# Kernel tuning notes

Measured on AMD Instinct MI355X. Metric: run time of the kernel, lower is better.

## Reference

```python
import jax, jax.numpy as jnp
import numpy as np

N = 50000
IN_DIM = 1024
HID = 64
HEADS = 4
OUT_DIM = 128
NEG_SLOPE = 0.2


def setup_inputs() -> dict:
    key = jax.random.key(0)
    ks = jax.random.split(key, 10)
    x = jax.random.normal(ks[0], (N, IN_DIM), dtype=jnp.float32)
    edge_index = jax.random.randint(ks[1], (2, 800000), 0, N, dtype=jnp.int64)
    # GATConv 1: input_dim -> hidden_dim, heads=HEADS, concat=True
    W1 = jax.random.normal(ks[2], (IN_DIM, HEADS * HID), dtype=jnp.float32) * (1.0 / np.sqrt(IN_DIM))
    att_src1 = jax.random.normal(ks[3], (HEADS, HID), dtype=jnp.float32) * 0.1
    att_dst1 = jax.random.normal(ks[4], (HEADS, HID), dtype=jnp.float32) * 0.1
    b1 = jnp.zeros((HEADS * HID,), dtype=jnp.float32)
    # GATConv 2: hidden_dim*heads -> output_dim, heads=1, concat=False
    W2 = jax.random.normal(ks[5], (HEADS * HID, OUT_DIM), dtype=jnp.float32) * (1.0 / np.sqrt(HEADS * HID))
    att_src2 = jax.random.normal(ks[6], (1, OUT_DIM), dtype=jnp.float32) * 0.1
    att_dst2 = jax.random.normal(ks[7], (1, OUT_DIM), dtype=jnp.float32) * 0.1
    b2 = jnp.zeros((OUT_DIM,), dtype=jnp.float32)
    return {"x": x, "edge_index": edge_index, "W1": W1, "att_src1": att_src1,
            "att_dst1": att_dst1, "b1": b1, "W2": W2, "att_src2": att_src2,
            "att_dst2": att_dst2, "b2": b2}


def _gat_conv(x, src, dst, W, a_src, a_dst, b, heads, concat):
    # x: [N, F_in]; src/dst: [E'] (self-loops already included)
    n = x.shape[0]
    h = (x @ W).reshape(n, heads, -1)                 # [N, H, D]
    # per-node attention halves (PyG style)
    alpha_s = jnp.sum(h * a_src[None], axis=-1)       # [N, H]
    alpha_d = jnp.sum(h * a_dst[None], axis=-1)       # [N, H]
    e = jax.nn.leaky_relu(alpha_s[src] + alpha_d[dst], NEG_SLOPE)  # [E', H]
    # segment softmax over incoming edges of each destination node
    m = jax.ops.segment_max(e, dst, num_segments=n)   # [N, H]
    m = jnp.where(jnp.isfinite(m), m, 0.0)
    e = jnp.exp(e - m[dst])
    s = jax.ops.segment_sum(e, dst, num_segments=n)   # [N, H]
    alpha = e / (s[dst] + 1e-16)                      # [E', H]
    out = jax.ops.segment_sum(h[src] * alpha[:, :, None], dst, num_segments=n)  # [N, H, D]
    out = out.reshape(n, -1) if concat else out.mean(axis=1)
    return out + b


def reference(x, edge_index, W1, att_src1, att_dst1, b1, W2, att_src2, att_dst2, b2):
    n = x.shape[0]
    # PyG GATConv default: add self-loops
    loops = jnp.arange(n, dtype=edge_index.dtype)
    src = jnp.concatenate([edge_index[0], loops])
    dst = jnp.concatenate([edge_index[1], loops])
    # dropout layers are identity in eval mode
    h = _gat_conv(x, src, dst, W1, att_src1, att_dst1, b1, HEADS, concat=True)
    h = jax.nn.elu(h)
    out = _gat_conv(h, src, dst, W2, att_src2, att_dst2, b2, 1, concat=False)
    # F.normalize(p=2, dim=-1)
    norm = jnp.maximum(jnp.linalg.norm(out, axis=-1, keepdims=True), 1e-12)
    return out / norm
```

## Files before the change

kernel.cpp:

```cpp
#include <hip/hip_runtime.h>
#include <math.h>

#define NNODES 50000
#define E0 800000
#define ETOT 850000
#define IN_DIM 1024
#define HEADS 4
#define C1 256
#define C2 128
#define NEG_SLOPE 0.2f

typedef short bf16x8 __attribute__((ext_vector_type(8)));
typedef float f32x4 __attribute__((ext_vector_type(4)));
typedef unsigned short ushort_t;

__device__ __forceinline__ void edge_sd(const int* __restrict__ ei, int e, int& s, int& d) {
    if (e < E0) { s = ei[e]; d = ei[E0 + e]; }
    else        { s = e - E0; d = s; }
}

__device__ __forceinline__ ushort_t f2b(float f) {
    unsigned u = __float_as_uint(f);
    return (ushort_t)((u + 0x7fffu + ((u >> 16) & 1u)) >> 16);
}
__device__ __forceinline__ float bf2f(ushort_t u) {
    return __uint_as_float((unsigned)u << 16);
}
__device__ __forceinline__ float lrelu(float v) { return v > 0.f ? v : NEG_SLOPE * v; }

__device__ __forceinline__ void gload_lds16(const void* g, void* l) {
    __builtin_amdgcn_global_load_lds(
        (const __attribute__((address_space(1))) unsigned int*)g,
        (__attribute__((address_space(3))) unsigned int*)l, 16, 0, 0);
}

__device__ __forceinline__ bf16x8 cvt_bf8(float4 f0, float4 f1) {
    bf16x8 p;
    p[0] = f2b(f0.x); p[1] = f2b(f0.y); p[2] = f2b(f0.z); p[3] = f2b(f0.w);
    p[4] = f2b(f1.x); p[5] = f2b(f1.y); p[6] = f2b(f1.z); p[7] = f2b(f1.w);
    return p;
}

__global__ __launch_bounds__(256) void wtrans_kernel(const float* __restrict__ W,
                                                     ushort_t* __restrict__ WT,
                                                     int K, int N)
{
    int idx = blockIdx.x * 256 + threadIdx.x;
    if (idx >= K * N) return;
    int k = idx / N, n = idx % N;
    WT[((size_t)(k >> 3) * N + n) * 8 + (k & 7)] = f2b(W[idx]);
}

__global__ __launch_bounds__(256, 4) void gemm_fb(const float* __restrict__ A,
                                                  const ushort_t* __restrict__ Bblk,
                                                  ushort_t* __restrict__ Cb,
                                                  int M, int N, int K)
{
    __shared__ __align__(16) ushort_t Bs[2][8 * 128 * 8];

    const int tid  = threadIdx.x;
    const int lane = tid & 63;
    const int wid  = tid >> 6;
    const int wr   = wid >> 1, wc = wid & 1;
    const int rowBase = blockIdx.y * 64;
    const int colBase = blockIdx.x * 128;
    const int r0 = lane & 15;
    const int kh = lane >> 4;

    const float* aP0 = A + (size_t)min(rowBase + wr * 32 + r0,      M - 1) * K + kh * 8;
    const float* aP1 = A + (size_t)min(rowBase + wr * 32 + 16 + r0, M - 1) * K + kh * 8;

    const int p0 = wid * 2;
    const ushort_t* bsrc0 = Bblk + ((size_t)(p0 + 0) * N + colBase + lane) * 8;
    const ushort_t* bsrc1 = Bblk + ((size_t)(p0 + 1) * N + colBase + lane) * 8;
    const int bdst0 = (p0 + 0) * 1024;
    const int bdst1 = (p0 + 1) * 1024;
    const size_t bstep = (size_t)8 * N * 8;

    const int brd = (wc * 64 + r0) * 8;

    f32x4 zero = {0.f, 0.f, 0.f, 0.f};
    f32x4 acc[2][4];
    #pragma unroll
    for (int i = 0; i < 2; ++i)
        #pragma unroll
        for (int j = 0; j < 4; ++j) acc[i][j] = zero;

    gload_lds16(bsrc0,       &Bs[0][bdst0]);
    gload_lds16(bsrc0 + 512, &Bs[0][bdst0 + 512]);
    gload_lds16(bsrc1,       &Bs[0][bdst1]);
    gload_lds16(bsrc1 + 512, &Bs[0][bdst1 + 512]);
    float4 n00 = *(const float4*)(aP0 +  0), n01 = *(const float4*)(aP0 +  4);
    float4 n02 = *(const float4*)(aP0 + 32), n03 = *(const float4*)(aP0 + 36);
    float4 n10 = *(const float4*)(aP1 +  0), n11 = *(const float4*)(aP1 +  4);
    float4 n12 = *(const float4*)(aP1 + 32), n13 = *(const float4*)(aP1 + 36);
    __syncthreads();

    const ushort_t* rdB = Bs[0];
    ushort_t*       stB = Bs[1];

    bf16x8 aC[2][2];
    aC[0][0] = cvt_bf8(n00, n01); aC[0][1] = cvt_bf8(n02, n03);
    aC[1][0] = cvt_bf8(n10, n11); aC[1][1] = cvt_bf8(n12, n13);

    const int nt = K >> 6;
    for (int t = 0; t < nt; ++t) {
        const int kt = (t + 1) << 6;
        const bool has_next = kt < K;
        if (has_next) {
            const ushort_t* b0 = bsrc0 + (size_t)(t + 1) * bstep;
            const ushort_t* b1 = bsrc1 + (size_t)(t + 1) * bstep;
            gload_lds16(b0,       stB + bdst0);
            gload_lds16(b0 + 512, stB + bdst0 + 512);
            gload_lds16(b1,       stB + bdst1);
            gload_lds16(b1 + 512, stB + bdst1 + 512);
            n00 = *(const float4*)(aP0 + kt +  0); n01 = *(const float4*)(aP0 + kt +  4);
            n02 = *(const float4*)(aP0 + kt + 32); n03 = *(const float4*)(aP0 + kt + 36);
            n10 = *(const float4*)(aP1 + kt +  0); n11 = *(const float4*)(aP1 + kt +  4);
            n12 = *(const float4*)(aP1 + kt + 32); n13 = *(const float4*)(aP1 + kt + 36);
        }

        #pragma unroll
        for (int kc = 0; kc < 2; ++kc) {
            const ushort_t* bbase = rdB + (kc * 4 + kh) * 1024 + brd;
            bf16x8 bF[4];
            #pragma unroll
            for (int fj = 0; fj < 4; ++fj) bF[fj] = *(const bf16x8*)(bbase + fj * 128);
            #pragma unroll
            for (int fi = 0; fi < 2; ++fi)
                #pragma unroll
                for (int fj = 0; fj < 4; ++fj)
                    acc[fi][fj] = __builtin_amdgcn_mfma_f32_16x16x32_bf16(
                        aC[fi][kc], bF[fj], acc[fi][fj], 0, 0, 0);
        }

        if (has_next) {
            aC[0][0] = cvt_bf8(n00, n01); aC[0][1] = cvt_bf8(n02, n03);
            aC[1][0] = cvt_bf8(n10, n11); aC[1][1] = cvt_bf8(n12, n13);
        }
        __syncthreads();
        ushort_t* tmp = (ushort_t*)rdB; rdB = stB; stB = tmp;
    }

    #pragma unroll
    for (int fi = 0; fi < 2; ++fi) {
        int row0 = rowBase + wr * 32 + fi * 16 + kh * 4;
        #pragma unroll
        for (int i = 0; i < 4; ++i) {
            int row = row0 + i;
            if (row < M) {
                #pragma unroll
                for (int fj = 0; fj < 4; ++fj)
                    Cb[(size_t)row * N + colBase + wc * 64 + fj * 16 + r0] = f2b(acc[fi][fj][i]);
            }
        }
    }
}

__global__ __launch_bounds__(256, 4) void gemm_bb(const ushort_t* __restrict__ Ab,
                                                  const ushort_t* __restrict__ Bblk,
                                                  ushort_t* __restrict__ Cb,
                                                  int M, int N, int K)
{
    __shared__ __align__(16) ushort_t Bs[2][8 * 128 * 8];

    const int tid  = threadIdx.x;
    const int lane = tid & 63;
    const int wid  = tid >> 6;
    const int wr   = wid >> 1, wc = wid & 1;
    const int rowBase = blockIdx.y * 64;
    const int colBase = blockIdx.x * 128;
    const int r0 = lane & 15;
    const int kh = lane >> 4;

    const ushort_t* aP0 = Ab + (size_t)min(rowBase + wr * 32 + r0,      M - 1) * K + kh * 8;
    const ushort_t* aP1 = Ab + (size_t)min(rowBase + wr * 32 + 16 + r0, M - 1) * K + kh * 8;

    const int p0 = wid * 2;
    const ushort_t* bsrc0 = Bblk + ((size_t)(p0 + 0) * N + colBase + lane) * 8;
    const ushort_t* bsrc1 = Bblk + ((size_t)(p0 + 1) * N + colBase + lane) * 8;
    const int bdst0 = (p0 + 0) * 1024;
    const int bdst1 = (p0 + 1) * 1024;
    const size_t bstep = (size_t)8 * N * 8;

    const int brd = (wc * 64 + r0) * 8;

    f32x4 zero = {0.f, 0.f, 0.f, 0.f};
    f32x4 acc[2][4];
    #pragma unroll
    for (int i = 0; i < 2; ++i)
        #pragma unroll
        for (int j = 0; j < 4; ++j) acc[i][j] = zero;

    gload_lds16(bsrc0,       &Bs[0][bdst0]);
    gload_lds16(bsrc0 + 512, &Bs[0][bdst0 + 512]);
    gload_lds16(bsrc1,       &Bs[0][bdst1]);
    gload_lds16(bsrc1 + 512, &Bs[0][bdst1 + 512]);
    bf16x8 aC[2][2], aN[2][2];
    aC[0][0] = *(const bf16x8*)(aP0 +  0); aC[0][1] = *(const bf16x8*)(aP0 + 32);
    aC[1][0] = *(const bf16x8*)(aP1 +  0); aC[1][1] = *(const bf16x8*)(aP1 + 32);
    __syncthreads();

    const ushort_t* rdB = Bs[0];
    ushort_t*       stB = Bs[1];

    const int nt = K >> 6;
    for (int t = 0; t < nt; ++t) {
        const int kt = (t + 1) << 6;
        const bool has_next = kt < K;
        if (has_next) {
            const ushort_t* b0 = bsrc0 + (size_t)(t + 1) * bstep;
            const ushort_t* b1 = bsrc1 + (size_t)(t + 1) * bstep;
            gload_lds16(b0,       stB + bdst0);
            gload_lds16(b0 + 512, stB + bdst0 + 512);
            gload_lds16(b1,       stB + bdst1);
            gload_lds16(b1 + 512, stB + bdst1 + 512);
            aN[0][0] = *(const bf16x8*)(aP0 + kt +  0); aN[0][1] = *(const bf16x8*)(aP0 + kt + 32);
            aN[1][0] = *(const bf16x8*)(aP1 + kt +  0); aN[1][1] = *(const bf16x8*)(aP1 + kt + 32);
        }

        #pragma unroll
        for (int kc = 0; kc < 2; ++kc) {
            const ushort_t* bbase = rdB + (kc * 4 + kh) * 1024 + brd;
            bf16x8 bF[4];
            #pragma unroll
            for (int fj = 0; fj < 4; ++fj) bF[fj] = *(const bf16x8*)(bbase + fj * 128);
            #pragma unroll
            for (int fi = 0; fi < 2; ++fi)
                #pragma unroll
                for (int fj = 0; fj < 4; ++fj)
                    acc[fi][fj] = __builtin_amdgcn_mfma_f32_16x16x32_bf16(
                        aC[fi][kc], bF[fj], acc[fi][fj], 0, 0, 0);
        }

        if (has_next) {
            aC[0][0] = aN[0][0]; aC[0][1] = aN[0][1];
            aC[1][0] = aN[1][0]; aC[1][1] = aN[1][1];
        }
        __syncthreads();
        ushort_t* tmp = (ushort_t*)rdB; rdB = stB; stB = tmp;
    }

    #pragma unroll
    for (int fi = 0; fi < 2; ++fi) {
        int row0 = rowBase + wr * 32 + fi * 16 + kh * 4;
        #pragma unroll
        for (int i = 0; i < 4; ++i) {
            int row = row0 + i;
            if (row < M) {
                #pragma unroll
                for (int fj = 0; fj < 4; ++fj)
                    Cb[(size_t)row * N + colBase + wc * 64 + fj * 16 + r0] = f2b(acc[fi][fj][i]);
            }
        }
    }
}

__global__ __launch_bounds__(256) void alpha1_kernel(const ushort_t* __restrict__ h1b,
                                                     const float* __restrict__ asrc,
                                                     const float* __restrict__ adst,
                                                     float* __restrict__ out_s,
                                                     float* __restrict__ out_d)
{
    int n = blockIdx.x;
    int t = threadIdx.x;
    float h = bf2f(h1b[(size_t)n * C1 + t]);
    float s = h * asrc[t];
    float d = h * adst[t];
    #pragma unroll
    for (int off = 32; off > 0; off >>= 1) {
        s += __shfl_down(s, off);
        d += __shfl_down(d, off);
    }
    if ((t & 63) == 0) {
        out_s[n * HEADS + (t >> 6)] = s;
        out_d[n * HEADS + (t >> 6)] = d;
    }
}

__global__ __launch_bounds__(64) void alpha2_kernel(const ushort_t* __restrict__ h2b,
                                                    const float* __restrict__ asrc,
                                                    const float* __restrict__ adst,
                                                    float* __restrict__ out_s,
                                                    float* __restrict__ out_d)
{
    int n = blockIdx.x;
    int t = threadIdx.x;
    float a = bf2f(h2b[(size_t)n * C2 + t]);
    float b = bf2f(h2b[(size_t)n * C2 + t + 64]);
    float s = a * asrc[t] + b * asrc[t + 64];
    float d = a * adst[t] + b * adst[t + 64];
    #pragma unroll
    for (int off = 32; off > 0; off >>= 1) {
        s += __shfl_down(s, off);
        d += __shfl_down(d, off);
    }
    if (t == 0) { out_s[n] = s; out_d[n] = d; }
}

__global__ __launch_bounds__(256) void deg_kernel(const int* __restrict__ ei,
                                                  int* __restrict__ deg)
{
    int e = blockIdx.x * blockDim.x + threadIdx.x;
    if (e >= ETOT) return;
    int s, d; edge_sd(ei, e, s, d);
    atomicAdd(&deg[d], 1);
}

#define SCAN_T 1024
__global__ __launch_bounds__(SCAN_T) void scan_kernel(const int* __restrict__ deg,
                                                      int* __restrict__ rowptr)
{
    __shared__ int wsum[16];
    __shared__ int chunk_tot;
    __shared__ int carry_s;
    const int t = threadIdx.x, lane = t & 63, w = t >> 6;
    if (t == 0) carry_s = 0;
    __syncthreads();
    for (int base = 0; base < NNODES; base += SCAN_T * 4) {
        int idx = base + t * 4;
        int v0 = (idx + 0 < NNODES) ? deg[idx + 0] : 0;
        int v1 = (idx + 1 < NNODES) ? deg[idx + 1] : 0;
        int v2 = (idx + 2 < NNODES) ? deg[idx + 2] : 0;
        int v3 = (idx + 3 < NNODES) ? deg[idx + 3] : 0;
        int p0 = v0, p1 = p0 + v1, p2 = p1 + v2, p3 = p2 + v3;
        int incl = p3;
        #pragma unroll
        for (int off = 1; off < 64; off <<= 1) {
            int nb = __shfl_up(incl, off);
            if (lane >= off) incl += nb;
        }
        if (lane == 63) wsum[w] = incl;
        __syncthreads();
        if (w == 0 && lane < 16) {
            int ws = wsum[lane];
            int wincl = ws;
            #pragma unroll
            for (int off = 1; off < 16; off <<= 1) {
                int nb = __shfl_up(wincl, off);
                if (lane >= off) wincl += nb;
            }
            wsum[lane] = wincl - ws;
            if (lane == 15) chunk_tot = wincl;
        }
        __syncthreads();
        int carry = carry_s;
        int basev = carry + wsum[w] + (incl - p3);
        if (idx + 0 < NNODES) rowptr[idx + 0] = basev;
        if (idx + 1 < NNODES) rowptr[idx + 1] = basev + p0;
        if (idx + 2 < NNODES) rowptr[idx + 2] = basev + p1;
        if (idx + 3 < NNODES) rowptr[idx + 3] = basev + p2;
        __syncthreads();
        if (t == 0) carry_s = carry + chunk_tot;
        __syncthreads();
    }
    if (threadIdx.x == 0) rowptr[NNODES] = carry_s;
}

__global__ __launch_bounds__(256) void scatter_kernel(const int* __restrict__ ei,
                                                      int* __restrict__ cursor,
                                                      int* __restrict__ srcs)
{
    int e = blockIdx.x * blockDim.x + threadIdx.x;
    if (e >= ETOT) return;
    int s, d; edge_sd(ei, e, s, d);
    int pos = atomicAdd(&cursor[d], 1);
    srcs[pos] = s;
}

__global__ __launch_bounds__(256) void weights1_kernel(const int* __restrict__ rowptr,
                                                       const int* __restrict__ srcs,
                                                       const float4* __restrict__ as1,
                                                       const float4* __restrict__ ad1,
                                                       float4* __restrict__ wbuf)
{
    int d = blockIdx.x * 4 + (threadIdx.x >> 6);
    if (d >= NNODES) return;
    int lane = threadIdx.x & 63;
    int beg = rowptr[d], end = rowptr[d + 1];
    float4 adv = ad1[d];
    float m0 = -INFINITY, m1 = -INFINITY, m2 = -INFINITY, m3 = -INFINITY;
    for (int i = beg + lane; i < end; i += 64) {
        int s = srcs[i];
        float4 av = as1[s];
        m0 = fmaxf(m0, lrelu(av.x + adv.x));
        m1 = fmaxf(m1, lrelu(av.y + adv.y));
        m2 = fmaxf(m2, lrelu(av.z + adv.z));
        m3 = fmaxf(m3, lrelu(av.w + adv.w));
    }
    #pragma unroll
    for (int off = 32; off > 0; off >>= 1) {
        m0 = fmaxf(m0, __shfl_xor(m0, off));
        m1 = fmaxf(m1, __shfl_xor(m1, off));
        m2 = fmaxf(m2, __shfl_xor(m2, off));
        m3 = fmaxf(m3, __shfl_xor(m3, off));
    }
    float s0 = 0.f, s1 = 0.f, s2 = 0.f, s3 = 0.f;
    for (int i = beg + lane; i < end; i += 64) {
        int s = srcs[i];
        float4 av = as1[s];
        float w0 = expf(lrelu(av.x + adv.x) - m0);
        float w1 = expf(lrelu(av.y + adv.y) - m1);
        float w2 = expf(lrelu(av.z + adv.z) - m2);
        float w3 = expf(lrelu(av.w + adv.w) - m3);
        wbuf[i] = make_float4(w0, w1, w2, w3);
        s0 += w0; s1 += w1; s2 += w2; s3 += w3;
    }
    #pragma unroll
    for (int off = 32; off > 0; off >>= 1) {
        s0 += __shfl_xor(s0, off);
        s1 += __shfl_xor(s1, off);
        s2 += __shfl_xor(s2, off);
        s3 += __shfl_xor(s3, off);
    }
    float i0 = 1.f / (s0 + 1e-16f), i1 = 1.f / (s1 + 1e-16f);
    float i2 = 1.f / (s2 + 1e-16f), i3 = 1.f / (s3 + 1e-16f);
    for (int i = beg + lane; i < end; i += 64) {
        float4 wv = wbuf[i];
        wbuf[i] = make_float4(wv.x * i0, wv.y * i1, wv.z * i2, wv.w * i3);
    }
}

__global__ __launch_bounds__(256) void weights2_kernel(const int* __restrict__ rowptr,
                                                       const int* __restrict__ srcs,
                                                       const float* __restrict__ as2,
                                                       const float* __restrict__ ad2,
                                                       float* __restrict__ wbuf)
{
    int d = blockIdx.x * 4 + (threadIdx.x >> 6);
    if (d >= NNODES) return;
    int lane = threadIdx.x & 63;
    int beg = rowptr[d], end = rowptr[d + 1];
    float adv = ad2[d];
    float m = -INFINITY;
    for (int i = beg + lane; i < end; i += 64)
        m = fmaxf(m, lrelu(as2[srcs[i]] + adv));
    #pragma unroll
    for (int off = 32; off > 0; off >>= 1) m = fmaxf(m, __shfl_xor(m, off));
    float sm = 0.f;
    for (int i = beg + lane; i < end; i += 64) {
        float w = expf(lrelu(as2[srcs[i]] + adv) - m);
        wbuf[i] = w;
        sm += w;
    }
    #pragma unroll
    for (int off = 32; off > 0; off >>= 1) sm += __shfl_xor(sm, off);
    float inv = 1.f / (sm + 1e-16f);
    for (int i = beg + lane; i < end; i += 64) wbuf[i] *= inv;
}

__global__ __launch_bounds__(256) void aggr1_csr(const int* __restrict__ rowptr,
                                                 const int* __restrict__ srcs,
                                                 const ushort_t* __restrict__ h1b,
                                                 const float* __restrict__ wbuf,
                                                 const float* __restrict__ b1,
                                                 ushort_t* __restrict__ out)
{
    int d = blockIdx.x * 4 + (threadIdx.x >> 6);
    if (d >= NNODES) return;
    int lane = threadIdx.x & 63;
    int c0 = lane * 4;
    int head = lane >> 4;
    int beg = rowptr[d], end = rowptr[d + 1];
    float a0 = 0.f, a1 = 0.f, a2 = 0.f, a3 = 0.f;
    int i = beg;
    for (; i + 1 < end; i += 2) {
        int s0 = srcs[i], s1 = srcs[i + 1];
        float w0 = wbuf[i * 4 + head], w1 = wbuf[i * 4 + 4 + head];
        ushort4 v0 = *(const ushort4*)(h1b + (size_t)s0 * C1 + c0);
        ushort4 v1 = *(const ushort4*)(h1b + (size_t)s1 * C1 + c0);
        a0 = fmaf(w0, bf2f(v0.x), a0); a1 = fmaf(w0, bf2f(v0.y), a1);
        a2 = fmaf(w0, bf2f(v0.z), a2); a3 = fmaf(w0, bf2f(v0.w), a3);
        a0 = fmaf(w1, bf2f(v1.x), a0); a1 = fmaf(w1, bf2f(v1.y), a1);
        a2 = fmaf(w1, bf2f(v1.z), a2); a3 = fmaf(w1, bf2f(v1.w), a3);
    }
    if (i < end) {
        int s0 = srcs[i];
        float w0 = wbuf[i * 4 + head];
        ushort4 v0 = *(const ushort4*)(h1b + (size_t)s0 * C1 + c0);
        a0 = fmaf(w0, bf2f(v0.x), a0); a1 = fmaf(w0, bf2f(v0.y), a1);
        a2 = fmaf(w0, bf2f(v0.z), a2); a3 = fmaf(w0, bf2f(v0.w), a3);
    }
    float4 bv = *(const float4*)(b1 + c0);
    float o0 = a0 + bv.x, o1 = a1 + bv.y, o2 = a2 + bv.z, o3 = a3 + bv.w;
    ushort4 r;
    r.x = f2b(o0 > 0.f ? o0 : (expf(o0) - 1.f));
    r.y = f2b(o1 > 0.f ? o1 : (expf(o1) - 1.f));
    r.z = f2b(o2 > 0.f ? o2 : (expf(o2) - 1.f));
    r.w = f2b(o3 > 0.f ? o3 : (expf(o3) - 1.f));
    *(ushort4*)(out + (size_t)d * C1 + c0) = r;
}

__global__ __launch_bounds__(256) void aggr2_csr(const int* __restrict__ rowptr,
                                                 const int* __restrict__ srcs,
                                                 const ushort_t* __restrict__ h2b,
                                                 const float* __restrict__ wbuf,
                                                 const float* __restrict__ b2,
                                                 float* __restrict__ out)
{
    int d = blockIdx.x * 4 + (threadIdx.x >> 6);
    if (d >= NNODES) return;
    int lane = threadIdx.x & 63;
    int c0 = lane * 2;
    int beg = rowptr[d], end = rowptr[d + 1];
    float a0 = 0.f, a1 = 0.f;
    int i = beg;
    for (; i + 1 < end; i += 2) {
        int s0 = srcs[i], s1 = srcs[i + 1];
        float w0 = wbuf[i], w1 = wbuf[i + 1];
        ushort2 v0 = *(const ushort2*)(h2b + (size_t)s0 * C2 + c0);
        ushort2 v1 = *(const ushort2*)(h2b + (size_t)s1 * C2 + c0);
        a0 = fmaf(w0, bf2f(v0.x), a0); a1 = fmaf(w0, bf2f(v0.y), a1);
        a0 = fmaf(w1, bf2f(v1.x), a0); a1 = fmaf(w1, bf2f(v1.y), a1);
    }
    if (i < end) {
        float w0 = wbuf[i];
        ushort2 v0 = *(const ushort2*)(h2b + (size_t)srcs[i] * C2 + c0);
        a0 = fmaf(w0, bf2f(v0.x), a0); a1 = fmaf(w0, bf2f(v0.y), a1);
    }
    float2 bv = *(const float2*)(b2 + c0);
    float o0 = a0 + bv.x, o1 = a1 + bv.y;
    float sq = o0 * o0 + o1 * o1;
    #pragma unroll
    for (int off = 32; off > 0; off >>= 1) sq += __shfl_xor(sq, off);
    float inv = 1.0f / fmaxf(sqrtf(sq), 1e-12f);
    float2 r = make_float2(o0 * inv, o1 * inv);
    *(float2*)(out + (size_t)d * C2 + c0) = r;
}

extern "C" void kernel_launch(void* const* d_in, const int* in_sizes, int n_in,
                              void* d_out, int out_size, void* d_ws, size_t ws_size,
                              hipStream_t stream)
{
    const float* x     = (const float*)d_in[0];
    const int*   ei    = (const int*)d_in[1];
    const float* W1    = (const float*)d_in[2];
    const float* asrc1 = (const float*)d_in[3];
    const float* adst1 = (const float*)d_in[4];
    const float* b1    = (const float*)d_in[5];
    const float* W2    = (const float*)d_in[6];
    const float* asrc2 = (const float*)d_in[7];
    const float* adst2 = (const float*)d_in[8];
    const float* b2    = (const float*)d_in[9];
    float* out = (float*)d_out;

    char* ws = (char*)d_ws;
    size_t off = 0;
    auto alloc = [&](size_t nbytes) {
        void* p = ws + off;
        off += (nbytes + 15) & ~(size_t)15;
        return p;
    };
    ushort_t* h1b    = (ushort_t*)alloc((size_t)NNODES * C1 * 2);
    ushort_t* act1b  = (ushort_t*)alloc((size_t)NNODES * C1 * 2);
    ushort_t* h2b    = (ushort_t*)alloc((size_t)NNODES * C2 * 2);
    ushort_t* W1blk  = (ushort_t*)alloc((size_t)C1 * IN_DIM * 2);
    ushort_t* W2blk  = (ushort_t*)alloc((size_t)C2 * C1 * 2);
    float*    as1    = (float*)alloc((size_t)NNODES * HEADS * 4);
    float*    ad1    = (float*)alloc((size_t)NNODES * HEADS * 4);
    float*    as2    = (float*)alloc((size_t)NNODES * 4);
    float*    ad2    = (float*)alloc((size_t)NNODES * 4);
    float*    wbuf1  = (float*)alloc((size_t)ETOT * HEADS * 4);
    float*    wbuf2  = (float*)alloc((size_t)ETOT * 4);
    int*      deg    = (int*)alloc((size_t)NNODES * 4);
    int*      rowptr = (int*)alloc((size_t)(NNODES + 1) * 4);
    int*      cursor = (int*)alloc((size_t)(NNODES + 1) * 4);
    int*      srcs   = (int*)alloc((size_t)ETOT * 4);

    const int eb = (ETOT + 255) / 256;
    const int nb4 = (NNODES + 3) / 4;

    wtrans_kernel<<<(IN_DIM * C1 + 255) / 256, 256, 0, stream>>>(W1, W1blk, IN_DIM, C1);
    wtrans_kernel<<<(C1 * C2 + 255) / 256, 256, 0, stream>>>(W2, W2blk, C1, C2);

    hipMemsetAsync(deg, 0, (size_t)NNODES * 4, stream);
    deg_kernel<<<eb, 256, 0, stream>>>(ei, deg);
    scan_kernel<<<1, SCAN_T, 0, stream>>>(deg, rowptr);
    hipMemcpyAsync(cursor, rowptr, (size_t)(NNODES + 1) * 4, hipMemcpyDeviceToDevice, stream);
    scatter_kernel<<<eb, 256, 0, stream>>>(ei, cursor, srcs);

    dim3 g1(C1 / 128, (NNODES + 63) / 64);
    gemm_fb<<<g1, 256, 0, stream>>>(x, W1blk, h1b, NNODES, C1, IN_DIM);
    alpha1_kernel<<<NNODES, 256, 0, stream>>>(h1b, asrc1, adst1, as1, ad1);
    weights1_kernel<<<nb4, 256, 0, stream>>>(rowptr, srcs, (const float4*)as1,
                                             (const float4*)ad1, (float4*)wbuf1);
    aggr1_csr<<<nb4, 256, 0, stream>>>(rowptr, srcs, h1b, wbuf1, b1, act1b);

    dim3 g2(C2 / 128, (NNODES + 63) / 64);
    gemm_bb<<<g2, 256, 0, stream>>>(act1b, W2blk, h2b, NNODES, C2, C1);
    alpha2_kernel<<<NNODES, 64, 0, stream>>>(h2b, asrc2, adst2, as2, ad2);
    weights2_kernel<<<nb4, 256, 0, stream>>>(rowptr, srcs, as2, ad2, wbuf2);
    aggr2_csr<<<nb4, 256, 0, stream>>>(rowptr, srcs, h2b, wbuf2, b2, out);
}
```

Before: 491.4 us.

## Triple-buffer B tiles and prefetch two K-steps ahead in fp32 GEMM

Replaces the double-buffered loop in gemm_fb with a three-stage LDS ring and two register sets of A, issuing loads two iterations ahead. Partial vmcnt waits and a raw s_barrier replace the full __syncthreads, so loads for step t+1 can stay in flight during compute. This costs more LDS and registers, so launch bounds drop occupancy from 4 to 3 blocks. The hand-placed vmcnt counts depend on exact load ordering, and a raw s_barrier without an LDS waitcnt could be fragile.

```diff
diff --git a/kernel.cpp b/kernel.cpp
--- a/kernel.cpp
+++ b/kernel.cpp
@@ -51,12 +51,12 @@
     WT[((size_t)(k >> 3) * N + n) * 8 + (k & 7)] = f2b(W[idx]);
 }
 
-__global__ __launch_bounds__(256, 4) void gemm_fb(const float* __restrict__ A,
+__global__ __launch_bounds__(256, 3) void gemm_fb(const float* __restrict__ A,
                                                   const ushort_t* __restrict__ Bblk,
                                                   ushort_t* __restrict__ Cb,
                                                   int M, int N, int K)
 {
-    __shared__ __align__(16) ushort_t Bs[2][8 * 128 * 8];
+    __shared__ __align__(16) ushort_t Bs[3][8 * 128 * 8];
 
     const int tid  = threadIdx.x;
     const int lane = tid & 63;
@@ -86,61 +86,86 @@
         #pragma unroll
         for (int j = 0; j < 4; ++j) acc[i][j] = zero;
 
-    gload_lds16(bsrc0,       &Bs[0][bdst0]);
-    gload_lds16(bsrc0 + 512, &Bs[0][bdst0 + 512]);
-    gload_lds16(bsrc1,       &Bs[0][bdst1]);
-    gload_lds16(bsrc1 + 512, &Bs[0][bdst1 + 512]);
-    float4 n00 = *(const float4*)(aP0 +  0), n01 = *(const float4*)(aP0 +  4);
-    float4 n02 = *(const float4*)(aP0 + 32), n03 = *(const float4*)(aP0 + 36);
-    float4 n10 = *(const float4*)(aP1 +  0), n11 = *(const float4*)(aP1 +  4);
-    float4 n12 = *(const float4*)(aP1 + 32), n13 = *(const float4*)(aP1 + 36);
-    __syncthreads();
-
-    const ushort_t* rdB = Bs[0];
-    ushort_t*       stB = Bs[1];
-
-    bf16x8 aC[2][2];
-    aC[0][0] = cvt_bf8(n00, n01); aC[0][1] = cvt_bf8(n02, n03);
-    aC[1][0] = cvt_bf8(n10, n11); aC[1][1] = cvt_bf8(n12, n13);
-
+    ushort_t* pCur = Bs[0];
+    ushort_t* pNxt = Bs[1];
+    ushort_t* pStg = Bs[2];
+
+    float4 ra[8], rb[8];
+    bf16x8 fA[2][2], fB[2][2];
     const int nt = K >> 6;
-    for (int t = 0; t < nt; ++t) {
-        const int kt = (t + 1) << 6;
-        const bool has_next = kt < K;
-        if (has_next) {
-            const ushort_t* b0 = bsrc0 + (size_t)(t + 1) * bstep;
-            const ushort_t* b1 = bsrc1 + (size_t)(t + 1) * bstep;
-            gload_lds16(b0,       stB + bdst0);
-            gload_lds16(b0 + 512, stB + bdst0 + 512);
-            gload_lds16(b1,       stB + bdst1);
-            gload_lds16(b1 + 512, stB + bdst1 + 512);
-            n00 = *(const float4*)(aP0 + kt +  0); n01 = *(const float4*)(aP0 + kt +  4);
-            n02 = *(const float4*)(aP0 + kt + 32); n03 = *(const float4*)(aP0 + kt + 36);
-            n10 = *(const float4*)(aP1 + kt +  0); n11 = *(const float4*)(aP1 + kt +  4);
-            n12 = *(const float4*)(aP1 + kt + 32); n13 = *(const float4*)(aP1 + kt + 36);
-        }
-
-        #pragma unroll
-        for (int kc = 0; kc < 2; ++kc) {
-            const ushort_t* bbase = rdB + (kc * 4 + kh) * 1024 + brd;
-            bf16x8 bF[4];
-            #pragma unroll
-            for (int fj = 0; fj < 4; ++fj) bF[fj] = *(const bf16x8*)(bbase + fj * 128);
-            #pragma unroll
-            for (int fi = 0; fi < 2; ++fi)
-                #pragma unroll
-                for (int fj = 0; fj < 4; ++fj)
-                    acc[fi][fj] = __builtin_amdgcn_mfma_f32_16x16x32_bf16(
-                        aC[fi][kc], bF[fj], acc[fi][fj], 0, 0, 0);
-        }
-
-        if (has_next) {
-            aC[0][0] = cvt_bf8(n00, n01); aC[0][1] = cvt_bf8(n02, n03);
-            aC[1][0] = cvt_bf8(n10, n11); aC[1][1] = cvt_bf8(n12, n13);
-        }
-        __syncthreads();
-        ushort_t* tmp = (ushort_t*)rdB; rdB = stB; stB = tmp;
-    }
+
+    gload_lds16(bsrc0,       pCur + bdst0);
+    gload_lds16(bsrc0 + 512, pCur + bdst0 + 512);
+    gload_lds16(bsrc1,       pCur + bdst1);
+    gload_lds16(bsrc1 + 512, pCur + bdst1 + 512);
+    ra[0] = *(const float4*)(aP0 +  0); ra[1] = *(const float4*)(aP0 +  4);
+    ra[2] = *(const float4*)(aP0 + 32); ra[3] = *(const float4*)(aP0 + 36);
+    ra[4] = *(const float4*)(aP1 +  0); ra[5] = *(const float4*)(aP1 +  4);
+    ra[6] = *(const float4*)(aP1 + 32); ra[7] = *(const float4*)(aP1 + 36);
+    {
+        const ushort_t* b0 = bsrc0 + bstep;
+        const ushort_t* b1 = bsrc1 + bstep;
+        gload_lds16(b0,       pNxt + bdst0);
+        gload_lds16(b0 + 512, pNxt + bdst0 + 512);
+        gload_lds16(b1,       pNxt + bdst1);
+        gload_lds16(b1 + 512, pNxt + bdst1 + 512);
+        rb[0] = *(const float4*)(aP0 + 64 +  0); rb[1] = *(const float4*)(aP0 + 64 +  4);
+        rb[2] = *(const float4*)(aP0 + 64 + 32); rb[3] = *(const float4*)(aP0 + 64 + 36);
+        rb[4] = *(const float4*)(aP1 + 64 +  0); rb[5] = *(const float4*)(aP1 + 64 +  4);
+        rb[6] = *(const float4*)(aP1 + 64 + 32); rb[7] = *(const float4*)(aP1 + 64 + 36);
+    }
+    asm volatile("s_waitcnt vmcnt(12)" ::: "memory");
+    fA[0][0] = cvt_bf8(ra[0], ra[1]); fA[0][1] = cvt_bf8(ra[2], ra[3]);
+    fA[1][0] = cvt_bf8(ra[4], ra[5]); fA[1][1] = cvt_bf8(ra[6], ra[7]);
+    __builtin_amdgcn_s_barrier();
+
+#define GEMM_STEP(T, RI, RC, FU, FF)                                            \
+    {                                                                           \
+        const int t2 = (T) + 2;                                                 \
+        const bool has2 = t2 < nt;                                              \
+        if (has2) {                                                             \
+            const ushort_t* b0 = bsrc0 + (size_t)t2 * bstep;                    \
+            const ushort_t* b1 = bsrc1 + (size_t)t2 * bstep;                    \
+            gload_lds16(b0,       pStg + bdst0);                                \
+            gload_lds16(b0 + 512, pStg + bdst0 + 512);                          \
+            gload_lds16(b1,       pStg + bdst1);                                \
+            gload_lds16(b1 + 512, pStg + bdst1 + 512);                          \
+            const float* a0 = aP0 + (t2 << 6);                                  \
+            const float* a1 = aP1 + (t2 << 6);                                  \
+            RI[0] = *(const float4*)(a0 +  0); RI[1] = *(const float4*)(a0 +  4);\
+            RI[2] = *(const float4*)(a0 + 32); RI[3] = *(const float4*)(a0 + 36);\
+            RI[4] = *(const float4*)(a1 +  0); RI[5] = *(const float4*)(a1 +  4);\
+            RI[6] = *(const float4*)(a1 + 32); RI[7] = *(const float4*)(a1 + 36);\
+        }                                                                       \
+        _Pragma("unroll")                                                       \
+        for (int kc = 0; kc < 2; ++kc) {                                        \
+            const ushort_t* bbase = pCur + (kc * 4 + kh) * 1024 + brd;          \
+            bf16x8 bF[4];                                                       \
+            _Pragma("unroll")                                                   \
+            for (int fj = 0; fj < 4; ++fj)                                      \
+                bF[fj] = *(const bf16x8*)(bbase + fj * 128);                    \
+            _Pragma("unroll")                                                   \
+            for (int fi = 0; fi < 2; ++fi)                                      \
+                _Pragma("unroll")                                               \
+                for (int fj = 0; fj < 4; ++fj)                                  \
+                    acc[fi][fj] = __builtin_amdgcn_mfma_f32_16x16x32_bf16(      \
+                        FU[fi][kc], bF[fj], acc[fi][fj], 0, 0, 0);              \
+        }                                                                       \
+        if ((T) + 1 < nt) {                                                     \
+            if (has2) asm volatile("s_waitcnt vmcnt(12)" ::: "memory");         \
+            else      asm volatile("s_waitcnt vmcnt(0)"  ::: "memory");         \
+            FF[0][0] = cvt_bf8(RC[0], RC[1]); FF[0][1] = cvt_bf8(RC[2], RC[3]); \
+            FF[1][0] = cvt_bf8(RC[4], RC[5]); FF[1][1] = cvt_bf8(RC[6], RC[7]); \
+            __builtin_amdgcn_s_barrier();                                       \
+        }                                                                       \
+        ushort_t* tmp = pCur; pCur = pNxt; pNxt = pStg; pStg = tmp;             \
+    }
+
+    for (int t = 0; t < nt; t += 2) {
+        GEMM_STEP(t,     ra, rb, fA, fB);
+        GEMM_STEP(t + 1, rb, ra, fB, fA);
+    }
+#undef GEMM_STEP
 
     #pragma unroll
     for (int fi = 0; fi < 2; ++fi) {
```

Result: slower. 510.0 us (+3.8%).

## Stage A tiles in LDS, read B directly from global; unroll CSR gathers by four

Applied to the files above, without the earlier changes.

Both GEMM kernels swap roles: the A operand is now loaded cooperatively in 256-wide K chunks, converted to bf16 and stored in LDS, while B fragments are read straight from global memory (and cache) instead of being staged via global_load_lds double buffering. This aims to coalesce the large fp32 A reads and cut per-k-step barriers, at the cost of a single-buffered LDS stage with two syncs per step, more registers (16 float4 staging), and occupancy lowered to 3. The aggregation kernels unroll the edge gather loop from 2 to 4 to keep more independent loads in flight.

```diff
diff --git a/kernel.cpp b/kernel.cpp
--- a/kernel.cpp
+++ b/kernel.cpp
@@ -28,12 +28,6 @@
 }
 __device__ __forceinline__ float lrelu(float v) { return v > 0.f ? v : NEG_SLOPE * v; }
 
-__device__ __forceinline__ void gload_lds16(const void* g, void* l) {
-    __builtin_amdgcn_global_load_lds(
-        (const __attribute__((address_space(1))) unsigned int*)g,
-        (__attribute__((address_space(3))) unsigned int*)l, 16, 0, 0);
-}
-
 __device__ __forceinline__ bf16x8 cvt_bf8(float4 f0, float4 f1) {
     bf16x8 p;
     p[0] = f2b(f0.x); p[1] = f2b(f0.y); p[2] = f2b(f0.z); p[3] = f2b(f0.w);
@@ -51,12 +45,12 @@
     WT[((size_t)(k >> 3) * N + n) * 8 + (k & 7)] = f2b(W[idx]);
 }
 
-__global__ __launch_bounds__(256, 4) void gemm_fb(const float* __restrict__ A,
+__global__ __launch_bounds__(256, 3) void gemm_fb(const float* __restrict__ A,
                                                   const ushort_t* __restrict__ Bblk,
                                                   ushort_t* __restrict__ Cb,
                                                   int M, int N, int K)
 {
-    __shared__ __align__(16) ushort_t Bs[2][8 * 128 * 8];
+    __shared__ __align__(16) ushort_t As[32 * 64 * 8];
 
     const int tid  = threadIdx.x;
     const int lane = tid & 63;
@@ -67,17 +61,14 @@
     const int r0 = lane & 15;
     const int kh = lane >> 4;
 
-    const float* aP0 = A + (size_t)min(rowBase + wr * 32 + r0,      M - 1) * K + kh * 8;
-    const float* aP1 = A + (size_t)min(rowBase + wr * 32 + 16 + r0, M - 1) * K + kh * 8;
-
-    const int p0 = wid * 2;
-    const ushort_t* bsrc0 = Bblk + ((size_t)(p0 + 0) * N + colBase + lane) * 8;
-    const ushort_t* bsrc1 = Bblk + ((size_t)(p0 + 1) * N + colBase + lane) * 8;
-    const int bdst0 = (p0 + 0) * 1024;
-    const int bdst1 = (p0 + 1) * 1024;
-    const size_t bstep = (size_t)8 * N * 8;
-
-    const int brd = (wc * 64 + r0) * 8;
+    const int srow = tid >> 2;
+    const int sq   = tid & 3;
+    const float* aSrc = A + (size_t)min(rowBase + srow, M - 1) * K + sq * 64;
+    ushort_t* aDst = As + (sq * 8) * 512 + srow * 8;
+
+    const ushort_t* bBase = Bblk + ((size_t)kh * N + colBase + wc * 64 + r0) * 8;
+
+    const ushort_t* aRd = As + kh * 512 + (wr * 32 + r0) * 8;
 
     f32x4 zero = {0.f, 0.f, 0.f, 0.f};
     f32x4 acc[2][4];
@@ -86,60 +77,39 @@
         #pragma unroll
         for (int j = 0; j < 4; ++j) acc[i][j] = zero;
 
-    gload_lds16(bsrc0,       &Bs[0][bdst0]);
-    gload_lds16(bsrc0 + 512, &Bs[0][bdst0 + 512]);
-    gload_lds16(bsrc1,       &Bs[0][bdst1]);
-    gload_lds16(bsrc1 + 512, &Bs[0][bdst1 + 512]);
-    float4 n00 = *(const float4*)(aP0 +  0), n01 = *(const float4*)(aP0 +  4);
-    float4 n02 = *(const float4*)(aP0 + 32), n03 = *(const float4*)(aP0 + 36);
-    float4 n10 = *(const float4*)(aP1 +  0), n11 = *(const float4*)(aP1 +  4);
-    float4 n12 = *(const float4*)(aP1 + 32), n13 = *(const float4*)(aP1 + 36);
-    __syncthreads();
-
-    const ushort_t* rdB = Bs[0];
-    ushort_t*       stB = Bs[1];
-
-    bf16x8 aC[2][2];
-    aC[0][0] = cvt_bf8(n00, n01); aC[0][1] = cvt_bf8(n02, n03);
-    aC[1][0] = cvt_bf8(n10, n11); aC[1][1] = cvt_bf8(n12, n13);
-
-    const int nt = K >> 6;
-    for (int t = 0; t < nt; ++t) {
-        const int kt = (t + 1) << 6;
-        const bool has_next = kt < K;
-        if (has_next) {
-            const ushort_t* b0 = bsrc0 + (size_t)(t + 1) * bstep;
-            const ushort_t* b1 = bsrc1 + (size_t)(t + 1) * bstep;
-            gload_lds16(b0,       stB + bdst0);
-            gload_lds16(b0 + 512, stB + bdst0 + 512);
-            gload_lds16(b1,       stB + bdst1);
-            gload_lds16(b1 + 512, stB + bdst1 + 512);
-            n00 = *(const float4*)(aP0 + kt +  0); n01 = *(const float4*)(aP0 + kt +  4);
-            n02 = *(const float4*)(aP0 + kt + 32); n03 = *(const float4*)(aP0 + kt + 36);
-            n10 = *(const float4*)(aP1 + kt +  0); n11 = *(const float4*)(aP1 + kt +  4);
-            n12 = *(const float4*)(aP1 + kt + 32); n13 = *(const float4*)(aP1 + kt + 36);
-        }
-
-        #pragma unroll
-        for (int kc = 0; kc < 2; ++kc) {
-            const ushort_t* bbase = rdB + (kc * 4 + kh) * 1024 + brd;
+    float4 st[16];
+    #pragma unroll
+    for (int i = 0; i < 16; ++i) st[i] = *(const float4*)(aSrc + i * 4);
+
+    const int nstep = K >> 8;
+    for (int s = 0; s < nstep; ++s) {
+        __syncthreads();
+        #pragma unroll
+        for (int j = 0; j < 8; ++j)
+            *(bf16x8*)(aDst + j * 512) = cvt_bf8(st[2 * j], st[2 * j + 1]);
+        __syncthreads();
+
+        if (s + 1 < nstep) {
+            const float* nsrc = aSrc + (size_t)(s + 1) * 256;
+            #pragma unroll
+            for (int i = 0; i < 16; ++i) st[i] = *(const float4*)(nsrc + i * 4);
+        }
+
+        #pragma unroll
+        for (int j = 0; j < 8; ++j) {
+            const ushort_t* bit = bBase + ((size_t)(s * 32 + j * 4) * N) * 8;
             bf16x8 bF[4];
             #pragma unroll
-            for (int fj = 0; fj < 4; ++fj) bF[fj] = *(const bf16x8*)(bbase + fj * 128);
-            #pragma unroll
-            for (int fi = 0; fi < 2; ++fi)
-                #pragma unroll
-                for (int fj = 0; fj < 4; ++fj)
-                    acc[fi][fj] = __builtin_amdgcn_mfma_f32_16x16x32_bf16(
-                        aC[fi][kc], bF[fj], acc[fi][fj], 0, 0, 0);
-        }
-
-        if (has_next) {
-            aC[0][0] = cvt_bf8(n00, n01); aC[0][1] = cvt_bf8(n02, n03);
-            aC[1][0] = cvt_bf8(n10, n11); aC[1][1] = cvt_bf8(n12, n13);
-        }
-        __syncthreads();
-        ushort_t* tmp = (ushort_t*)rdB; rdB = stB; stB = tmp;
+            for (int fj = 0; fj < 4; ++fj)
+                bF[fj] = *(const bf16x8*)(bit + (size_t)fj * 128);
+            bf16x8 aF0 = *(const bf16x8*)(aRd + j * 2048);
+            bf16x8 aF1 = *(const bf16x8*)(aRd + j * 2048 + 128);
+            #pragma unroll
+            for (int fj = 0; fj < 4; ++fj) {
+                acc[0][fj] = __builtin_amdgcn_mfma_f32_16x16x32_bf16(aF0, bF[fj], acc[0][fj], 0, 0, 0);
+                acc[1][fj] = __builtin_amdgcn_mfma_f32_16x16x32_bf16(aF1, bF[fj], acc[1][fj], 0, 0, 0);
+            }
+        }
     }
 
     #pragma unroll
@@ -162,7 +132,7 @@
                                                   ushort_t* __restrict__ Cb,
                                                   int M, int N, int K)
 {
-    __shared__ __align__(16) ushort_t Bs[2][8 * 128 * 8];
+    __shared__ __align__(16) ushort_t As[32 * 64 * 8];
 
     const int tid  = threadIdx.x;
     const int lane = tid & 63;
@@ -173,17 +143,13 @@
     const int r0 = lane & 15;
     const int kh = lane >> 4;
 
-    const ushort_t* aP0 = Ab + (size_t)min(rowBase + wr * 32 + r0,      M - 1) * K + kh * 8;
-    const ushort_t* aP1 = Ab + (size_t)min(rowBase + wr * 32 + 16 + r0, M - 1) * K + kh * 8;
-
-    const int p0 = wid * 2;
-    const ushort_t* bsrc0 = Bblk + ((size_t)(p0 + 0) * N + colBase + lane) * 8;
-    const ushort_t* bsrc1 = Bblk + ((size_t)(p0 + 1) * N + colBase + lane) * 8;
-    const int bdst0 = (p0 + 0) * 1024;
-    const int bdst1 = (p0 + 1) * 1024;
-    const size_t bstep = (size_t)8 * N * 8;
-
-    const int brd = (wc * 64 + r0) * 8;
+    const int srow = tid >> 2;
+    const int sq   = tid & 3;
+    const ushort_t* aSrc = Ab + (size_t)min(rowBase + srow, M - 1) * K + sq * 64;
+    ushort_t* aDst = As + (sq * 8) * 512 + srow * 8;
+
+    const ushort_t* bBase = Bblk + ((size_t)kh * N + colBase + wc * 64 + r0) * 8;
+    const ushort_t* aRd = As + kh * 512 + (wr * 32 + r0) * 8;
 
     f32x4 zero = {0.f, 0.f, 0.f, 0.f};
     f32x4 acc[2][4];
@@ -192,53 +158,39 @@
         #pragma unroll
         for (int j = 0; j < 4; ++j) acc[i][j] = zero;
 
-    gload_lds16(bsrc0,       &Bs[0][bdst0]);
-    gload_lds16(bsrc0 + 512, &Bs[0][bdst0 + 512]);
-    gload_lds16(bsrc1,       &Bs[0][bdst1]);
-    gload_lds16(bsrc1 + 512, &Bs[0][bdst1 + 512]);
-    bf16x8 aC[2][2], aN[2][2];
-    aC[0][0] = *(const bf16x8*)(aP0 +  0); aC[0][1] = *(const bf16x8*)(aP0 + 32);
-    aC[1][0] = *(const bf16x8*)(aP1 +  0); aC[1][1] = *(const bf16x8*)(aP1 + 32);
-    __syncthreads();
-
-    const ushort_t* rdB = Bs[0];
-    ushort_t*       stB = Bs[1];
-
-    const int nt = K >> 6;
-    for (int t = 0; t < nt; ++t) {
-        const int kt = (t + 1) << 6;
-        const bool has_next = kt < K;
-        if (has_next) {
-            const ushort_t* b0 = bsrc0 + (size_t)(t + 1) * bstep;
-            const ushort_t* b1 = bsrc1 + (size_t)(t + 1) * bstep;
-            gload_lds16(b0,       stB + bdst0);
-            gload_lds16(b0 + 512, stB + bdst0 + 512);
-            gload_lds16(b1,       stB + bdst1);
-            gload_lds16(b1 + 512, stB + bdst1 + 512);
-            aN[0][0] = *(const bf16x8*)(aP0 + kt +  0); aN[0][1] = *(const bf16x8*)(aP0 + kt + 32);
-            aN[1][0] = *(const bf16x8*)(aP1 + kt +  0); aN[1][1] = *(const bf16x8*)(aP1 + kt + 32);
-        }
-
-        #pragma unroll
-        for (int kc = 0; kc < 2; ++kc) {
-            const ushort_t* bbase = rdB + (kc * 4 + kh) * 1024 + brd;
+    bf16x8 st[8];
+    #pragma unroll
+    for (int j = 0; j < 8; ++j) st[j] = *(const bf16x8*)(aSrc + j * 8);
+
+    const int nstep = K >> 8;
+    for (int s = 0; s < nstep; ++s) {
+        __syncthreads();
+        #pragma unroll
+        for (int j = 0; j < 8; ++j)
+            *(bf16x8*)(aDst + j * 512) = st[j];
+        __syncthreads();
+
+        if (s + 1 < nstep) {
+            const ushort_t* nsrc = aSrc + (size_t)(s + 1) * 256;
+            #pragma unroll
+            for (int j = 0; j < 8; ++j) st[j] = *(const bf16x8*)(nsrc + j * 8);
+        }
+
+        #pragma unroll
+        for (int j = 0; j < 8; ++j) {
+            const ushort_t* bit = bBase + ((size_t)(s * 32 + j * 4) * N) * 8;
             bf16x8 bF[4];
             #pragma unroll
-            for (int fj = 0; fj < 4; ++fj) bF[fj] = *(const bf16x8*)(bbase + fj * 128);
-            #pragma unroll
-            for (int fi = 0; fi < 2; ++fi)
-                #pragma unroll
-                for (int fj = 0; fj < 4; ++fj)
-                    acc[fi][fj] = __builtin_amdgcn_mfma_f32_16x16x32_bf16(
-                        aC[fi][kc], bF[fj], acc[fi][fj], 0, 0, 0);
-        }
-
-        if (has_next) {
-            aC[0][0] = aN[0][0]; aC[0][1] = aN[0][1];
-            aC[1][0] = aN[1][0]; aC[1][1] = aN[1][1];
-        }
-        __syncthreads();
-        ushort_t* tmp = (ushort_t*)rdB; rdB = stB; stB = tmp;
+            for (int fj = 0; fj < 4; ++fj)
+                bF[fj] = *(const bf16x8*)(bit + (size_t)fj * 128);
+            bf16x8 aF0 = *(const bf16x8*)(aRd + j * 2048);
+            bf16x8 aF1 = *(const bf16x8*)(aRd + j * 2048 + 128);
+            #pragma unroll
+            for (int fj = 0; fj < 4; ++fj) {
+                acc[0][fj] = __builtin_amdgcn_mfma_f32_16x16x32_bf16(aF0, bF[fj], acc[0][fj], 0, 0, 0);
+                acc[1][fj] = __builtin_amdgcn_mfma_f32_16x16x32_bf16(aF1, bF[fj], acc[1][fj], 0, 0, 0);
+            }
+        }
     }
 
     #pragma unroll
@@ -464,17 +416,24 @@
     int beg = rowptr[d], end = rowptr[d + 1];
     float a0 = 0.f, a1 = 0.f, a2 = 0.f, a3 = 0.f;
     int i = beg;
-    for (; i + 1 < end; i += 2) {
-        int s0 = srcs[i], s1 = srcs[i + 1];
-        float w0 = wbuf[i * 4 + head], w1 = wbuf[i * 4 + 4 + head];
+    for (; i + 3 < end; i += 4) {
+        int s0 = srcs[i], s1 = srcs[i + 1], s2 = srcs[i + 2], s3 = srcs[i + 3];
+        float w0 = wbuf[i * 4 + head],     w1 = wbuf[i * 4 + 4 + head];
+        float w2 = wbuf[i * 4 + 8 + head], w3 = wbuf[i * 4 + 12 + head];
         ushort4 v0 = *(const ushort4*)(h1b + (size_t)s0 * C1 + c0);
         ushort4 v1 = *(const ushort4*)(h1b + (size_t)s1 * C1 + c0);
+        ushort4 v2 = *(const ushort4*)(h1b + (size_t)s2 * C1 + c0);
+        ushort4 v3 = *(const ushort4*)(h1b + (size_t)s3 * C1 + c0);
         a0 = fmaf(w0, bf2f(v0.x), a0); a1 = fmaf(w0, bf2f(v0.y), a1);
         a2 = fmaf(w0, bf2f(v0.z), a2); a3 = fmaf(w0, bf2f(v0.w), a3);
         a0 = fmaf(w1, bf2f(v1.x), a0); a1 = fmaf(w1, bf2f(v1.y), a1);
         a2 = fmaf(w1, bf2f(v1.z), a2); a3 = fmaf(w1, bf2f(v1.w), a3);
-    }
-    if (i < end) {
+        a0 = fmaf(w2, bf2f(v2.x), a0); a1 = fmaf(w2, bf2f(v2.y), a1);
+        a2 = fmaf(w2, bf2f(v2.z), a2); a3 = fmaf(w2, bf2f(v2.w), a3);
+        a0 = fmaf(w3, bf2f(v3.x), a0); a1 = fmaf(w3, bf2f(v3.y), a1);
+        a2 = fmaf(w3, bf2f(v3.z), a2); a3 = fmaf(w3, bf2f(v3.w), a3);
+    }
+    for (; i < end; ++i) {
         int s0 = srcs[i];
         float w0 = wbuf[i * 4 + head];
         ushort4 v0 = *(const ushort4*)(h1b + (size_t)s0 * C1 + c0);
@@ -505,15 +464,19 @@
     int beg = rowptr[d], end = rowptr[d + 1];
     float a0 = 0.f, a1 = 0.f;
     int i = beg;
-    for (; i + 1 < end; i += 2) {
-        int s0 = srcs[i], s1 = srcs[i + 1];
-        float w0 = wbuf[i], w1 = wbuf[i + 1];
+    for (; i + 3 < end; i += 4) {
+        int s0 = srcs[i], s1 = srcs[i + 1], s2 = srcs[i + 2], s3 = srcs[i + 3];
+        float w0 = wbuf[i], w1 = wbuf[i + 1], w2 = wbuf[i + 2], w3 = wbuf[i + 3];
         ushort2 v0 = *(const ushort2*)(h2b + (size_t)s0 * C2 + c0);
         ushort2 v1 = *(const ushort2*)(h2b + (size_t)s1 * C2 + c0);
+        ushort2 v2 = *(const ushort2*)(h2b + (size_t)s2 * C2 + c0);
+        ushort2 v3 = *(const ushort2*)(h2b + (size_t)s3 * C2 + c0);
         a0 = fmaf(w0, bf2f(v0.x), a0); a1 = fmaf(w0, bf2f(v0.y), a1);
         a0 = fmaf(w1, bf2f(v1.x), a0); a1 = fmaf(w1, bf2f(v1.y), a1);
-    }
-    if (i < end) {
+        a0 = fmaf(w2, bf2f(v2.x), a0); a1 = fmaf(w2, bf2f(v2.y), a1);
+        a0 = fmaf(w3, bf2f(v3.x), a0); a1 = fmaf(w3, bf2f(v3.y), a1);
+    }
+    for (; i < end; ++i) {
         float w0 = wbuf[i];
         ushort2 v0 = *(const ushort2*)(h2b + (size_t)srcs[i] * C2 + c0);
         a0 = fmaf(w0, bf2f(v0.x), a0); a1 = fmaf(w0, bf2f(v0.y), a1);
```

Result: no change. 484.7 us (-1.4%).
